# Optimization experiments

Hardware: AMD Instinct MI355X
Metric: run time of the kernel (lower is better)

Reference implementation:

```python
import jax, jax.numpy as jnp
import numpy as np

B, Q, KV = 4, 256, 1024
QS, KS, H, VS = 128, 128, 128, 256

def setup_inputs() -> dict:
    key = jax.random.key(0)
    ks = jax.random.split(key, 7)
    return {
        "queries": jax.random.normal(ks[0], (B, Q, QS), dtype=jnp.float32),
        "keys": jax.random.normal(ks[1], (B, KV, KS), dtype=jnp.float32),
        "values": jax.random.normal(ks[2], (B, KV, VS), dtype=jnp.float32),
        "valid_lens": jax.random.randint(ks[3], (B,), 0, KV, dtype=jnp.int64 if jax.config.read('jax_enable_x64') else jnp.int32),
        "Wq": jax.random.normal(ks[4], (QS, H), dtype=jnp.float32),
        "Wk": jax.random.normal(ks[5], (KS, H), dtype=jnp.float32),
        "wv": jax.random.normal(ks[6], (H,), dtype=jnp.float32),
    }

def reference(queries, keys, values, valid_lens, Wq, Wk, wv):
    # project: [B,Q,H], [B,KV,H]
    q = jnp.einsum('bqd,dh->bqh', queries, Wq)
    k = jnp.einsum('bkd,dh->bkh', keys, Wk)
    # additive scores: broadcast add -> tanh -> reduce with w_v  [B,Q,KV]
    feats = jnp.tanh(q[:, :, None, :] + k[:, None, :, :])  # [B,Q,KV,H]
    scores = jnp.einsum('bqkh,h->bqk', feats, wv)
    # masked softmax over KV with value -1e6 at masked slots
    mask = jnp.arange(scores.shape[-1])[None, None, :] < valid_lens[:, None, None]
    scores = jnp.where(mask, scores, -1e6)
    attn = jax.nn.softmax(scores, axis=-1)
    # weighted sum of values  [B,Q,VS]
    return jnp.einsum('bqk,bkv->bqv', attn, values)
```

## Files before the change

### kernel.cpp

```cpp
#include <hip/hip_runtime.h>

#define C2LOG2E 2.8853900817779268f
#define LOG2E   1.4426950408889634f

__device__ __forceinline__ float sig2(float x) {
    return __builtin_amdgcn_rcpf(__builtin_amdgcn_exp2f(x) + 1.0f);
}

__global__ __launch_bounds__(256) void proj_kernel(
    const float* __restrict__ q_in, const float* __restrict__ k_in,
    const float* __restrict__ Wq, const float* __restrict__ Wk,
    const int* __restrict__ valid_lens,
    float* __restrict__ qc, float* __restrict__ kct)
{
    __shared__ __align__(16) float x_s[8][128];
    __shared__ __align__(16) float ps[4][8][128];
    int tid = threadIdx.x;
    int blk = blockIdx.x;
    bool is_q = (blk < 128);
    int r0 = (is_q ? blk : blk - 128) * 8;
    int bb = r0 >> 10;
    if (!is_q) {
        int vl = valid_lens[bb];
        if ((r0 & 1023) >= vl) return;
    }
    const float* X = (is_q ? q_in : k_in) + (size_t)r0 * 128;
    const float* W = is_q ? Wq : Wk;

    *(float4*)&x_s[tid >> 5][(tid & 31) * 4] = ((const float4*)X)[tid];
    __syncthreads();

    int hl = tid & 63;
    int dq = tid >> 6;
    float a0[8] = {0,0,0,0,0,0,0,0};
    float a1[8] = {0,0,0,0,0,0,0,0};
#pragma unroll
    for (int i4 = 0; i4 < 8; ++i4) {
        int d = dq*32 + i4*4;
        float w00 = W[(d+0)*128 + hl], w01 = W[(d+0)*128 + hl + 64];
        float w10 = W[(d+1)*128 + hl], w11 = W[(d+1)*128 + hl + 64];
        float w20 = W[(d+2)*128 + hl], w21 = W[(d+2)*128 + hl + 64];
        float w30 = W[(d+3)*128 + hl], w31 = W[(d+3)*128 + hl + 64];
#pragma unroll
        for (int r = 0; r < 8; ++r) {
            float4 xv = *(const float4*)&x_s[r][d];
            a0[r] = fmaf(xv.x,w00, fmaf(xv.y,w10, fmaf(xv.z,w20, fmaf(xv.w,w30, a0[r]))));
            a1[r] = fmaf(xv.x,w01, fmaf(xv.y,w11, fmaf(xv.z,w21, fmaf(xv.w,w31, a1[r]))));
        }
    }
#pragma unroll
    for (int r = 0; r < 8; ++r) {
        ps[dq][r][hl]      = a0[r];
        ps[dq][r][hl + 64] = a1[r];
    }
    __syncthreads();

    int r  = tid >> 5;
    int c4 = (tid & 31) * 4;
    float4 s0 = *(const float4*)&ps[0][r][c4];
    float4 s1 = *(const float4*)&ps[1][r][c4];
    float4 s2 = *(const float4*)&ps[2][r][c4];
    float4 s3 = *(const float4*)&ps[3][r][c4];
    float4 v = make_float4(((s0.x+s1.x)+(s2.x+s3.x))*C2LOG2E,
                           ((s0.y+s1.y)+(s2.y+s3.y))*C2LOG2E,
                           ((s0.z+s1.z)+(s2.z+s3.z))*C2LOG2E,
                           ((s0.w+s1.w)+(s2.w+s3.w))*C2LOG2E);
    if (is_q) {
        *(float4*)&qc[(size_t)(r0 + r)*128 + c4] = v;
    } else {
        int c    = (r0 & 1023) >> 6;
        int kvin = (r0 & 63) + r;
        *(float4*)&kct[((((size_t)(bb*16 + c))*32 + (c4 >> 2))*64 + kvin)*4] = v;
    }
}

__global__ __launch_bounds__(512, 8) void attn_split_kernel(
    const float* __restrict__ qc, const float* __restrict__ kct,
    const float* __restrict__ values, const int* __restrict__ valid_lens,
    const float* __restrict__ wv, float* __restrict__ pO, float* __restrict__ pml)
{
    __shared__ float2 e2_s[2][256];
    __shared__ float4 po[8][4][64];
    __shared__ float2 red_m[8], red_s[8];

    int tid  = threadIdx.x;
    int b    = blockIdx.y;
    int q0   = blockIdx.x * 4;
    int s    = blockIdx.z;
    int w    = tid >> 6;
    int lane = tid & 63;
    int qh   = w >> 2;
    int c    = w & 3;
    int vl   = valid_lens[b];
    int row0 = b*256 + q0;

    if (vl > 0 && s*256 >= vl) {
        if (tid < 4) pml[(size_t)(s*1024 + row0 + tid)*2] = -1e30f;
        return;
    }

    const float4* qa4 = (const float4*)(qc + (size_t)(row0 + 2*qh)*128);
    const float4* qb4 = qa4 + 32;
    const float4* wv4 = (const float4*)wv;
    int chunk = s*4 + c;
    const float4* p0 = (const float4*)kct + ((size_t)(b*16 + chunk))*2048 + lane;

    float a00 = 0.f, a10 = 0.f;
    if (chunk*64 < vl) {
#pragma unroll 4
        for (int hb = 0; hb < 32; ++hb) {
            float4 wvv = wv4[hb];
            float4 qa = qa4[hb], qb = qb4[hb];
            float4 k0 = p0[(size_t)hb*64];
            a00 = fmaf(wvv.x, sig2(qa.x + k0.x), a00);
            a10 = fmaf(wvv.x, sig2(qb.x + k0.x), a10);
            a00 = fmaf(wvv.y, sig2(qa.y + k0.y), a00);
            a10 = fmaf(wvv.y, sig2(qb.y + k0.y), a10);
            a00 = fmaf(wvv.z, sig2(qa.z + k0.z), a00);
            a10 = fmaf(wvv.z, sig2(qb.z + k0.z), a10);
            a00 = fmaf(wvv.w, sig2(qa.w + k0.w), a00);
            a10 = fmaf(wvv.w, sig2(qb.w + k0.w), a10);
        }
    }

    int lkv = c*64 + lane;
    bool valid = (s*256 + lkv < vl);
    float s00 = valid ? -2.f*a00 : -1e6f;
    float s10 = valid ? -2.f*a10 : -1e6f;

    float m0 = s00, m1 = s10;
#pragma unroll
    for (int off = 32; off; off >>= 1) {
        m0 = fmaxf(m0, __shfl_xor(m0, off));
        m1 = fmaxf(m1, __shfl_xor(m1, off));
    }
    if (lane == 0) red_m[w] = make_float2(m0, m1);
    __syncthreads();
    {
        float2 mm = red_m[qh*4];
#pragma unroll
        for (int ww = 1; ww < 4; ++ww) {
            float2 t = red_m[qh*4 + ww];
            mm.x = fmaxf(mm.x, t.x); mm.y = fmaxf(mm.y, t.y);
        }
        m0 = mm.x; m1 = mm.y;
    }

    float e00 = __builtin_amdgcn_exp2f((s00 - m0) * LOG2E);
    float e10 = __builtin_amdgcn_exp2f((s10 - m1) * LOG2E);
    e2_s[qh][lkv] = make_float2(e00, e10);
    float l0 = e00, l1 = e10;
#pragma unroll
    for (int off = 32; off; off >>= 1) {
        l0 += __shfl_xor(l0, off);
        l1 += __shfl_xor(l1, off);
    }
    if (lane == 0) red_s[w] = make_float2(l0, l1);
    __syncthreads();

    int local_end = (vl == 0) ? 256 : min(256, vl - s*256);
    float4 ac[4] = {{0,0,0,0},{0,0,0,0},{0,0,0,0},{0,0,0,0}};
    const float4* V4 = (const float4*)values + (size_t)b*65536 + (size_t)s*256*64 + lane;
#pragma unroll 2
    for (int k2 = w; k2 < local_end; k2 += 8) {
        float4 vv = V4[(size_t)k2*64];
        float2 ea = e2_s[0][k2];
        float2 eb = e2_s[1][k2];
        ac[0].x = fmaf(ea.x, vv.x, ac[0].x); ac[0].y = fmaf(ea.x, vv.y, ac[0].y);
        ac[0].z = fmaf(ea.x, vv.z, ac[0].z); ac[0].w = fmaf(ea.x, vv.w, ac[0].w);
        ac[1].x = fmaf(ea.y, vv.x, ac[1].x); ac[1].y = fmaf(ea.y, vv.y, ac[1].y);
        ac[1].z = fmaf(ea.y, vv.z, ac[1].z); ac[1].w = fmaf(ea.y, vv.w, ac[1].w);
        ac[2].x = fmaf(eb.x, vv.x, ac[2].x); ac[2].y = fmaf(eb.x, vv.y, ac[2].y);
        ac[2].z = fmaf(eb.x, vv.z, ac[2].z); ac[2].w = fmaf(eb.x, vv.w, ac[2].w);
        ac[3].x = fmaf(eb.y, vv.x, ac[3].x); ac[3].y = fmaf(eb.y, vv.y, ac[3].y);
        ac[3].z = fmaf(eb.y, vv.z, ac[3].z); ac[3].w = fmaf(eb.y, vv.w, ac[3].w);
    }
#pragma unroll
    for (int q = 0; q < 4; ++q) po[w][q][lane] = ac[q];

    if (tid < 4) {
        int rqh = tid >> 1;
        float mm = -1e30f, lsum = 0.f;
#pragma unroll
        for (int ww = 0; ww < 4; ++ww) {
            float2 tm = red_m[rqh*4 + ww];
            float2 tl = red_s[rqh*4 + ww];
            mm   = fmaxf(mm, (tid & 1) ? tm.y : tm.x);
            lsum += (tid & 1) ? tl.y : tl.x;
        }
        *(float2*)&pml[(size_t)(s*1024 + row0 + tid)*2] = make_float2(mm, lsum);
    }
    __syncthreads();

    int qq  = tid >> 7;
    int col = (tid & 127) * 2;
    const float* pp = (const float*)po;
    float rx = 0.f, ry = 0.f;
#pragma unroll
    for (int ww = 0; ww < 8; ++ww) {
        float2 p = *(const float2*)&pp[(ww*4 + qq)*256 + col];
        rx += p.x; ry += p.y;
    }
    *(float2*)&pO[(size_t)(s*1024 + row0 + qq)*256 + col] = make_float2(rx, ry);
}

__global__ __launch_bounds__(256) void combine_kernel(
    const float* __restrict__ pO, const float* __restrict__ pml,
    float* __restrict__ out)
{
    int tid  = threadIdx.x;
    int row  = blockIdx.x*4 + (tid >> 6);
    int lane = tid & 63;
    float2 ml[4];
    float m = -1e30f;
#pragma unroll
    for (int s = 0; s < 4; ++s) {
        ml[s] = *(const float2*)&pml[(size_t)(s*1024 + row)*2];
        m = fmaxf(m, ml[s].x);
    }
    float ws[4], denom = 0.f;
#pragma unroll
    for (int s = 0; s < 4; ++s) {
        ws[s] = __builtin_amdgcn_exp2f((ml[s].x - m) * LOG2E);
        denom = fmaf(ws[s], ml[s].y, denom);
    }
    float inv = 1.0f / denom;
    float4 o = {0,0,0,0};
#pragma unroll
    for (int s = 0; s < 4; ++s) {
        float4 os = ((const float4*)pO)[(size_t)(s*1024 + row)*64 + lane];
        o.x = fmaf(ws[s], os.x, o.x); o.y = fmaf(ws[s], os.y, o.y);
        o.z = fmaf(ws[s], os.z, o.z); o.w = fmaf(ws[s], os.w, o.w);
    }
    o.x *= inv; o.y *= inv; o.z *= inv; o.w *= inv;
    ((float4*)out)[(size_t)row*64 + lane] = o;
}

extern "C" void kernel_launch(void* const* d_in, const int* in_sizes, int n_in,
                              void* d_out, int out_size, void* d_ws, size_t ws_size,
                              hipStream_t stream)
{
    const float* queries = (const float*)d_in[0];
    const float* keys    = (const float*)d_in[1];
    const float* values  = (const float*)d_in[2];
    const int*   vlens   = (const int*)d_in[3];
    const float* Wq      = (const float*)d_in[4];
    const float* Wk      = (const float*)d_in[5];
    const float* wv      = (const float*)d_in[6];
    float* out = (float*)d_out;

    float* qc  = (float*)d_ws;
    float* kct = qc  + 4*256*128;
    float* pO  = kct + 4*16*32*64*4;
    float* pml = pO  + 4*1024*256;

    proj_kernel<<<640, 256, 0, stream>>>(queries, keys, Wq, Wk, vlens, qc, kct);
    attn_split_kernel<<<dim3(64, 4, 4), 512, 0, stream>>>(qc, kct, values, vlens, wv, pO, pml);
    combine_kernel<<<256, 256, 0, stream>>>(pO, pml, out);
}
```

Measured before the change: 99.95 us.

## Interleave KV positions across splits to balance work under valid_lens masking

Split s now owns the strided KV positions 4*j+s instead of a contiguous 256-wide block, and the projection kernel writes the transposed K with a matching permutation. The early-exit for splits lying entirely past valid_len is removed, so every split does a similar amount of work and the masked tail no longer leaves whole blocks idle while others do full work. The trade-off is strided value reads (stride of four rows) and loss of the cheap skip for fully masked splits. The pml write is also moved before the value loop, and the wave index goes through readfirstlane so it is treated as wave-uniform.

```diff
diff --git a/kernel.cpp b/kernel.cpp
--- a/kernel.cpp
+++ b/kernel.cpp
@@ -68,9 +68,9 @@
     if (is_q) {
         *(float4*)&qc[(size_t)(r0 + r)*128 + c4] = v;
     } else {
-        int c    = (r0 & 1023) >> 6;
-        int kvin = (r0 & 63) + r;
-        *(float4*)&kct[((((size_t)(bb*16 + c))*32 + (c4 >> 2))*64 + kvin)*4] = v;
+        int kvl = (r0 & 1023) + r;
+        int p   = (kvl & 3)*256 + (kvl >> 2);
+        *(float4*)&kct[((((size_t)(bb*16 + (p >> 6)))*32 + (c4 >> 2))*64 + (p & 63))*4] = v;
     }
 }
 
@@ -81,32 +81,27 @@
 {
     __shared__ float2 e2_s[2][256];
     __shared__ float4 po[8][4][64];
-    __shared__ float2 red_m[8], red_s[8];
+    __shared__ float2 red_m[2][4], red_s[2][4];
 
     int tid  = threadIdx.x;
+    int w    = __builtin_amdgcn_readfirstlane(tid) >> 6;
+    int lane = tid & 63;
     int b    = blockIdx.y;
     int q0   = blockIdx.x * 4;
     int s    = blockIdx.z;
-    int w    = tid >> 6;
-    int lane = tid & 63;
-    int qh   = w >> 2;
-    int c    = w & 3;
     int vl   = valid_lens[b];
     int row0 = b*256 + q0;
 
-    if (vl > 0 && s*256 >= vl) {
-        if (tid < 4) pml[(size_t)(s*1024 + row0 + tid)*2] = -1e30f;
-        return;
-    }
+    int qh = w >> 2;
+    int c  = w & 3;
 
     const float4* qa4 = (const float4*)(qc + (size_t)(row0 + 2*qh)*128);
     const float4* qb4 = qa4 + 32;
     const float4* wv4 = (const float4*)wv;
-    int chunk = s*4 + c;
-    const float4* p0 = (const float4*)kct + ((size_t)(b*16 + chunk))*2048 + lane;
+    const float4* p0  = (const float4*)kct + ((size_t)(b*16 + s*4 + c))*2048 + lane;
 
     float a00 = 0.f, a10 = 0.f;
-    if (chunk*64 < vl) {
+    if (c*256 + s < vl) {
 #pragma unroll 4
         for (int hb = 0; hb < 32; ++hb) {
             float4 wvv = wv4[hb];
@@ -123,8 +118,8 @@
         }
     }
 
-    int lkv = c*64 + lane;
-    bool valid = (s*256 + lkv < vl);
+    int j = c*64 + lane;
+    bool valid = (4*j + s < vl);
     float s00 = valid ? -2.f*a00 : -1e6f;
     float s10 = valid ? -2.f*a10 : -1e6f;
 
@@ -134,13 +129,13 @@
         m0 = fmaxf(m0, __shfl_xor(m0, off));
         m1 = fmaxf(m1, __shfl_xor(m1, off));
     }
-    if (lane == 0) red_m[w] = make_float2(m0, m1);
+    if (lane == 0) red_m[qh][c] = make_float2(m0, m1);
     __syncthreads();
     {
-        float2 mm = red_m[qh*4];
-#pragma unroll
-        for (int ww = 1; ww < 4; ++ww) {
-            float2 t = red_m[qh*4 + ww];
+        float2 mm = red_m[qh][0];
+#pragma unroll
+        for (int cc = 1; cc < 4; ++cc) {
+            float2 t = red_m[qh][cc];
             mm.x = fmaxf(mm.x, t.x); mm.y = fmaxf(mm.y, t.y);
         }
         m0 = mm.x; m1 = mm.y;
@@ -148,22 +143,35 @@
 
     float e00 = __builtin_amdgcn_exp2f((s00 - m0) * LOG2E);
     float e10 = __builtin_amdgcn_exp2f((s10 - m1) * LOG2E);
-    e2_s[qh][lkv] = make_float2(e00, e10);
+    e2_s[qh][j] = make_float2(e00, e10);
     float l0 = e00, l1 = e10;
 #pragma unroll
     for (int off = 32; off; off >>= 1) {
         l0 += __shfl_xor(l0, off);
         l1 += __shfl_xor(l1, off);
     }
-    if (lane == 0) red_s[w] = make_float2(l0, l1);
-    __syncthreads();
-
-    int local_end = (vl == 0) ? 256 : min(256, vl - s*256);
+    if (lane == 0) red_s[qh][c] = make_float2(l0, l1);
+    __syncthreads();
+
+    if (tid < 4) {
+        int rqh = tid >> 1;
+        float mm = -1e30f, lsum = 0.f;
+#pragma unroll
+        for (int cc = 0; cc < 4; ++cc) {
+            float2 tm = red_m[rqh][cc];
+            float2 tl = red_s[rqh][cc];
+            mm   = fmaxf(mm, (tid & 1) ? tm.y : tm.x);
+            lsum += (tid & 1) ? tl.y : tl.x;
+        }
+        *(float2*)&pml[(size_t)(s*1024 + row0 + tid)*2] = make_float2(mm, lsum);
+    }
+
+    int local_end = (vl == 0) ? 256 : min(256, (vl - s + 3) >> 2);
     float4 ac[4] = {{0,0,0,0},{0,0,0,0},{0,0,0,0},{0,0,0,0}};
-    const float4* V4 = (const float4*)values + (size_t)b*65536 + (size_t)s*256*64 + lane;
+    const float4* V4 = (const float4*)values + (size_t)b*65536 + (size_t)s*64 + lane;
 #pragma unroll 2
     for (int k2 = w; k2 < local_end; k2 += 8) {
-        float4 vv = V4[(size_t)k2*64];
+        float4 vv = V4[(size_t)k2*256];
         float2 ea = e2_s[0][k2];
         float2 eb = e2_s[1][k2];
         ac[0].x = fmaf(ea.x, vv.x, ac[0].x); ac[0].y = fmaf(ea.x, vv.y, ac[0].y);
@@ -177,19 +185,6 @@
     }
 #pragma unroll
     for (int q = 0; q < 4; ++q) po[w][q][lane] = ac[q];
-
-    if (tid < 4) {
-        int rqh = tid >> 1;
-        float mm = -1e30f, lsum = 0.f;
-#pragma unroll
-        for (int ww = 0; ww < 4; ++ww) {
-            float2 tm = red_m[rqh*4 + ww];
-            float2 tl = red_s[rqh*4 + ww];
-            mm   = fmaxf(mm, (tid & 1) ? tm.y : tm.x);
-            lsum += (tid & 1) ? tl.y : tl.x;
-        }
-        *(float2*)&pml[(size_t)(s*1024 + row0 + tid)*2] = make_float2(mm, lsum);
-    }
     __syncthreads();
 
     int qq  = tid >> 7;
```

Result: slower. 103.0 us (+3.1%).
